# Performance work log

Measured on AMD Instinct MI355X. Metric: run time of the kernel, lower is better.

## Reference

```python
import jax, jax.numpy as jnp
import numpy as np

B, A, D = 1024, 200, 128
H = 8
DH = D // H
TANH_CLIP = 10.0


def setup_inputs() -> dict:
    key = jax.random.key(0)
    k = jax.random.split(key, 8)
    agent_embd = jax.random.normal(k[0], (B, A, D), dtype=jnp.float32)
    # old_action must be a permutation per row (no revisits under the mask)
    old_action = jax.vmap(lambda kk: jax.random.permutation(kk, A))(
        jax.random.split(k[1], B)).astype(jnp.int32)
    s = 0.02
    W_placeholder = jax.random.uniform(k[2], (D,), jnp.float32, -1.0, 1.0)
    W_node = jax.random.normal(k[3], (D, 3 * D), jnp.float32) * s   # project_node_embeddings
    W_fixed = jax.random.normal(k[4], (D, D), jnp.float32) * s      # project_fixed_context
    W_step = jax.random.normal(k[5], (D, D), jnp.float32) * s       # project_step_context
    W_out = jax.random.normal(k[6], (D, D), jnp.float32) * s        # project_out
    return {"agent_embd": agent_embd, "old_action": old_action,
            "W_placeholder": W_placeholder, "W_node": W_node,
            "W_fixed": W_fixed, "W_step": W_step, "W_out": W_out}


def _decode(agent_embd, old_action, W_placeholder, W_node, W_fixed, W_step, W_out):
    b_, a_, d_ = agent_embd.shape
    inv_sqrt_dh = np.float32(1.0 / np.sqrt(DH))
    inv_sqrt_d = np.float32(1.0 / np.sqrt(d_))
    batch_ix = jnp.arange(b_)

    # _precompute: fixed context + per-head K/V + logit keys
    graph_embed = agent_embd.mean(axis=1)                      # [B, D]
    fixed_ctx = graph_embed @ W_fixed                          # [B, D]
    proj = agent_embd @ W_node                                 # [B, A, 3D]
    gK, gV, logit_K = jnp.split(proj, 3, axis=-1)              # each [B, A, D]
    gK = gK.reshape(b_, a_, H, DH).transpose(2, 0, 1, 3)       # [H, B, A, dh]
    gV = gV.reshape(b_, a_, H, DH).transpose(2, 0, 1, 3)       # [H, B, A, dh]

    def step(carry, xs):
        mask, prev = carry                                     # [B, A] bool, [B] int
        i, act = xs
        gathered = agent_embd[batch_ix, prev]                  # [B, D]
        step_ctx = jnp.where(i == 0, W_placeholder[None, :], gathered)
        query = fixed_ctx + step_ctx @ W_step                  # [B, D]
        mask = jnp.where(i > 0, mask.at[batch_ix, prev].set(True), mask)

        Q = query.reshape(b_, H, DH).transpose(1, 0, 2)        # [H, B, dh]
        compat = jnp.einsum('hbd,hbad->hba', Q, gK) * inv_sqrt_dh
        compat = jnp.where(mask[None, :, :], -jnp.inf, compat)  # mask_inner
        attn = jax.nn.softmax(compat, axis=-1)                 # [H, B, A]
        heads = jnp.einsum('hba,hbad->hbd', attn, gV)          # [H, B, dh]
        glimpse = heads.transpose(1, 0, 2).reshape(b_, d_) @ W_out  # [B, D]

        logits = jnp.einsum('bd,bad->ba', glimpse, logit_K) * inv_sqrt_d
        logits = jnp.tanh(logits) * TANH_CLIP
        logits = jnp.where(mask, -jnp.inf, logits)             # mask_logits
        log_p = jax.nn.log_softmax(logits, axis=-1)            # [B, A]
        lp_sel = log_p[batch_ix, act]                          # [B]
        return (mask, act), lp_sel

    mask0 = jnp.zeros((b_, a_), dtype=bool)
    prev0 = jnp.zeros((b_,), dtype=old_action.dtype)
    xs = (jnp.arange(a_), old_action.T)
    _, lps = jax.lax.scan(step, (mask0, prev0), xs)            # lps: [A, B]
    return old_action, lps.sum(axis=0)


def reference(agent_embd, old_action, W_placeholder, W_node, W_fixed, W_step, W_out):
    return _decode(agent_embd, old_action, W_placeholder, W_node, W_fixed, W_step, W_out)
```

## Files before the change

### kernel.cpp

```cpp
#include <hip/hip_runtime.h>
#include <cstdint>
#include <cstddef>

#define BB 1024
#define AA 200
#define DD 128
#define HH 8
#define N3 384

typedef unsigned short u16;
typedef unsigned int u32;
typedef __attribute__((ext_vector_type(8))) short bf16x8;
typedef __attribute__((ext_vector_type(4))) float f32x4;

__device__ __forceinline__ float bf2f(u16 v){ return __uint_as_float(((u32)v) << 16); }
__device__ __forceinline__ u16 f2bf(float f){
  u32 u = __float_as_uint(f);
  u32 r = u + 0x7fffu + ((u >> 16) & 1u);
  return (u16)(r >> 16);
}
__device__ __forceinline__ u32 pack2(float lo, float hi){
  return (u32)f2bf(lo) | ((u32)f2bf(hi) << 16);
}
__device__ __forceinline__ u32 pack2t(float lo, float hi){
  return (__float_as_uint(hi) & 0xFFFF0000u) | (__float_as_uint(lo) >> 16);
}
__device__ __forceinline__ bf16x8 pack8(float4 a, float4 b){
  bf16x8 o;
  o[0] = (short)f2bf(a.x); o[1] = (short)f2bf(a.y);
  o[2] = (short)f2bf(a.z); o[3] = (short)f2bf(a.w);
  o[4] = (short)f2bf(b.x); o[5] = (short)f2bf(b.y);
  o[6] = (short)f2bf(b.z); o[7] = (short)f2bf(b.w);
  return o;
}

__global__ void k_act_rank(const int* __restrict__ oa, float* __restrict__ out0,
                           int* __restrict__ rank){
  int m = blockIdx.x * 256 + threadIdx.x;
  if (m >= BB*AA) return;
  int v = oa[m];
  out0[m] = (float)v;
  int b = m / AA;
  int j = m - b*AA;
  rank[b*AA + v] = j;
}

__global__ void k_prep(const float* __restrict__ Wn, const float* __restrict__ Ws,
                       const float* __restrict__ Wo,
                       u16* __restrict__ WnT, u16* __restrict__ WsT,
                       u16* __restrict__ WoT){
  int idx = blockIdx.x * 256 + threadIdx.x;
  if (idx < 49152){
    int n = idx >> 7, k = idx & 127;
    WnT[idx] = f2bf(Wn[k*N3 + n]);
  } else if (idx < 65536){
    int j = idx - 49152;
    int n = j >> 7, k = j & 127;
    WsT[j] = f2bf(Ws[k*DD + n]);
  } else if (idx < 81920){
    int j = idx - 65536;
    int n = j >> 7, k = j & 127;
    WoT[j] = f2bf(Wo[k*DD + n]);
  }
}

__global__ void k_fixed(const float* __restrict__ E, const float* __restrict__ Wf,
                        float* __restrict__ fixedc){
  int b = blockIdx.x;
  int d = threadIdx.x;
  __shared__ float ge[DD];
  const float* Eb = E + (size_t)b*AA*DD;
  float s = 0.f;
  for (int a = 0; a < AA; ++a) s += Eb[a*DD + d];
  ge[d] = s * (1.0f/AA);
  __syncthreads();
  float acc = 0.f;
  for (int k = 0; k < DD; ++k) acc = fmaf(ge[k], Wf[k*DD + d], acc);
  fixedc[b*DD + d] = acc;
}

__global__ __launch_bounds__(256) void k_proj_mfma(const float* __restrict__ E,
                                                   const u16* __restrict__ WnT,
                                                   u16* __restrict__ proj){
  const int t = threadIdx.x;
  const int w = t >> 6, L = t & 63;
  const int l16 = L & 15, lq = L >> 4;
  const int m0 = blockIdx.x * 128;
  const int n0 = blockIdx.y * 128;
  const int row0 = m0 + w*32;

  f32x4 acc[2][8] = {};
  const float* Arow0 = E + (size_t)(row0 + l16)*DD;
  const float* Arow1 = Arow0 + (size_t)16*DD;
  #pragma unroll
  for (int ks = 0; ks < 4; ++ks){
    int ko = ks*32 + lq*8;
    bf16x8 a0 = pack8(*(const float4*)(Arow0 + ko), *(const float4*)(Arow0 + ko + 4));
    bf16x8 a1 = pack8(*(const float4*)(Arow1 + ko), *(const float4*)(Arow1 + ko + 4));
    #pragma unroll
    for (int nt = 0; nt < 8; ++nt){
      union { uint4 u; bf16x8 v; } bb;
      bb.u = *(const uint4*)(WnT + (size_t)(n0 + nt*16 + l16)*DD + ko);
      acc[0][nt] = __builtin_amdgcn_mfma_f32_16x16x32_bf16(a0, bb.v, acc[0][nt], 0, 0, 0);
      acc[1][nt] = __builtin_amdgcn_mfma_f32_16x16x32_bf16(a1, bb.v, acc[1][nt], 0, 0, 0);
    }
  }
  #pragma unroll
  for (int mt = 0; mt < 2; ++mt)
    #pragma unroll
    for (int r = 0; r < 4; ++r){
      int row = row0 + mt*16 + lq*4 + r;
      u16* dst = proj + (size_t)row*N3 + n0;
      #pragma unroll
      for (int nt = 0; nt < 8; ++nt)
        dst[nt*16 + l16] = f2bf(acc[mt][nt][r]);
    }
}

__global__ __launch_bounds__(256) void k_query_mfma(const float* __restrict__ E,
                                                    const int* __restrict__ oa,
                                                    const float* __restrict__ Wp,
                                                    const u16* __restrict__ WsT,
                                                    const float* __restrict__ fixedc,
                                                    u16* __restrict__ qhg){
  const int t = threadIdx.x;
  const int w = t >> 6, L = t & 63;
  const int l16 = L & 15, lq = L >> 4;
  const int m0 = blockIdx.x * 128;
  const int row0 = m0 + w*32;

  const float* src[2];
  #pragma unroll
  for (int mt = 0; mt < 2; ++mt){
    int q = row0 + mt*16 + l16;
    int b = q / AA, i = q - b*AA;
    src[mt] = (i == 0) ? Wp : (E + (size_t)(b*AA + oa[b*AA + i - 1])*DD);
  }

  f32x4 acc[2][8] = {};
  #pragma unroll
  for (int ks = 0; ks < 4; ++ks){
    int ko = ks*32 + lq*8;
    bf16x8 a0 = pack8(*(const float4*)(src[0] + ko), *(const float4*)(src[0] + ko + 4));
    bf16x8 a1 = pack8(*(const float4*)(src[1] + ko), *(const float4*)(src[1] + ko + 4));
    #pragma unroll
    for (int nt = 0; nt < 8; ++nt){
      union { uint4 u; bf16x8 v; } bb;
      bb.u = *(const uint4*)(WsT + (size_t)(nt*16 + l16)*DD + ko);
      acc[0][nt] = __builtin_amdgcn_mfma_f32_16x16x32_bf16(a0, bb.v, acc[0][nt], 0, 0, 0);
      acc[1][nt] = __builtin_amdgcn_mfma_f32_16x16x32_bf16(a1, bb.v, acc[1][nt], 0, 0, 0);
    }
  }
  #pragma unroll
  for (int mt = 0; mt < 2; ++mt)
    #pragma unroll
    for (int r = 0; r < 4; ++r){
      int row = row0 + mt*16 + lq*4 + r;
      int b = row / AA;
      const float* fc = fixedc + (size_t)b*DD;
      u16* dst = qhg + (size_t)row*DD;
      #pragma unroll
      for (int nt = 0; nt < 8; ++nt)
        dst[nt*16 + l16] = f2bf((acc[mt][nt][r] + fc[nt*16 + l16]) * 0.25f);
    }
}

#define KSTR 24
#define VSTR 232
template<int IT>
__device__ __forceinline__ void attn_tile(const u16* KL, const u16* VT,
                                          u16* Qbase, int l16, int lq,
                                          bool dm0, bool dm1, bool dm2, bool dm3){
  constexpr int NT = 13 - IT;
  const int qi = IT*16 + l16;
  const float NEG_INF = -__builtin_inff();

  union { uint4 u; bf16x8 v; } qf8;
  qf8.u.x = 0; qf8.u.y = 0; qf8.u.z = 0; qf8.u.w = 0;
  if (qi < AA){
    uint2 q2 = *(const uint2*)(Qbase + (size_t)qi*DD + lq*4);
    qf8.u.x = q2.x; qf8.u.y = q2.y;
  }

  f32x4 S[NT];
  #pragma unroll
  for (int k = 0; k < NT; ++k){
    const int at = IT + k;
    union { uint4 u; bf16x8 v; } kf8;
    uint2 k2 = *(const uint2*)&KL[(at*16 + l16)*KSTR + lq*4];
    kf8.u.x = k2.x; kf8.u.y = k2.y; kf8.u.z = 0; kf8.u.w = 0;
    f32x4 z = {0.f,0.f,0.f,0.f};
    S[k] = __builtin_amdgcn_mfma_f32_16x16x32_bf16(kf8.v, qf8.v, z, 0, 0, 0);
  }
  S[0][0] = dm0 ? NEG_INF : S[0][0];
  S[0][1] = dm1 ? NEG_INF : S[0][1];
  S[0][2] = dm2 ? NEG_INF : S[0][2];
  S[0][3] = dm3 ? NEG_INF : S[0][3];
  if (lq >= 2){
    S[NT-1][0] = NEG_INF; S[NT-1][1] = NEG_INF;
    S[NT-1][2] = NEG_INF; S[NT-1][3] = NEG_INF;
  }
  float m = fmaxf(fmaxf(S[0][0], S[0][1]), fmaxf(S[0][2], S[0][3]));
  #pragma unroll
  for (int k = 1; k < NT; ++k)
    m = fmaxf(m, fmaxf(fmaxf(S[k][0], S[k][1]), fmaxf(S[k][2], S[k][3])));
  m = fmaxf(m, __shfl_xor(m, 16));
  m = fmaxf(m, __shfl_xor(m, 32));
  m = fmaxf(m, -1e30f);
  float s0 = 0.f, s1 = 0.f, s2 = 0.f, s3 = 0.f;
  #pragma unroll
  for (int k = 0; k < NT; ++k){
    float e0 = __expf(S[k][0] - m);
    float e1 = __expf(S[k][1] - m);
    float e2 = __expf(S[k][2] - m);
    float e3 = __expf(S[k][3] - m);
    S[k][0] = e0; S[k][1] = e1; S[k][2] = e2; S[k][3] = e3;
    s0 += e0; s1 += e1; s2 += e2; s3 += e3;
  }
  float sum = (s0 + s1) + (s2 + s3);
  sum += __shfl_xor(sum, 16);
  sum += __shfl_xor(sum, 32);
  float inv = 1.0f / sum;
  f32x4 acc = {0.f,0.f,0.f,0.f};
  #pragma unroll
  for (int k = 0; k < NT; ++k){
    const int at = IT + k;
    union { uint4 u; bf16x8 v; } pa8, vb8;
    pa8.u.x = pack2t(S[k][0], S[k][1]);
    pa8.u.y = pack2t(S[k][2], S[k][3]);
    pa8.u.z = 0; pa8.u.w = 0;
    uint2 v2 = *(const uint2*)&VT[l16*VSTR + at*16 + lq*4];
    vb8.u.x = v2.x; vb8.u.y = v2.y; vb8.u.z = 0; vb8.u.w = 0;
    acc = __builtin_amdgcn_mfma_f32_16x16x32_bf16(vb8.v, pa8.v, acc, 0, 0, 0);
  }
  if (qi < AA){
    uint2 ov;
    ov.x = pack2(acc[0]*inv, acc[1]*inv);
    ov.y = pack2(acc[2]*inv, acc[3]*inv);
    *(uint2*)(Qbase + (size_t)qi*DD + lq*4) = ov;
  }
}

__global__ __launch_bounds__(256) void k_attn(const u16* __restrict__ proj,
                                              const int* __restrict__ oa,
                                              u16* __restrict__ qhg){
  __shared__ __align__(16) u16 KL[208*KSTR];
  __shared__ __align__(16) u16 VT[16*VSTR];
  const int b = blockIdx.x;
  const int h = blockIdx.y;
  const int t = threadIdx.x;
  const int w = t >> 6, L = t & 63;
  const int l16 = L & 15, lq = L >> 4;

  if (t < 192) KL[200*KSTR + t] = 0;
  if (t < 128){ int d = t >> 3, c = t & 7; VT[d*VSTR + 200 + c] = 0; }

  if (t < AA){
    int a = oa[(size_t)b*AA + t];
    const u16* src = proj + ((size_t)(b*AA + a))*N3 + h*16;
    uint4 k0 = *(const uint4*)(src);
    uint4 k1 = *(const uint4*)(src + 8);
    *(uint4*)&KL[t*KSTR]     = k0;
    *(uint4*)&KL[t*KSTR + 8] = k1;
    const u16* sv = src + 128;
    u16 d16[16];
    *(uint4*)(d16)   = *(const uint4*)(sv);
    *(uint4*)(d16+8) = *(const uint4*)(sv+8);
    #pragma unroll
    for (int d = 0; d < 16; ++d) VT[d*VSTR + t] = d16[d];
  }
  __syncthreads();

  u16* Qbase = qhg + (size_t)b*AA*DD + h*16;
  const bool dm0 = (lq*4 + 0) < l16;
  const bool dm1 = (lq*4 + 1) < l16;
  const bool dm2 = (lq*4 + 2) < l16;
  const bool dm3 = (lq*4 + 3) < l16;

  if (w == 0){
    attn_tile<0>(KL, VT, Qbase, l16, lq, dm0, dm1, dm2, dm3);
    attn_tile<3>(KL, VT, Qbase, l16, lq, dm0, dm1, dm2, dm3);
  } else if (w == 1){
    attn_tile<1>(KL, VT, Qbase, l16, lq, dm0, dm1, dm2, dm3);
    attn_tile<2>(KL, VT, Qbase, l16, lq, dm0, dm1, dm2, dm3);
  } else if (w == 2){
    attn_tile<4>(KL, VT, Qbase, l16, lq, dm0, dm1, dm2, dm3);
    attn_tile<6>(KL, VT, Qbase, l16, lq, dm0, dm1, dm2, dm3);
    attn_tile<8>(KL, VT, Qbase, l16, lq, dm0, dm1, dm2, dm3);
    attn_tile<10>(KL, VT, Qbase, l16, lq, dm0, dm1, dm2, dm3);
    attn_tile<12>(KL, VT, Qbase, l16, lq, dm0, dm1, dm2, dm3);
  } else {
    attn_tile<5>(KL, VT, Qbase, l16, lq, dm0, dm1, dm2, dm3);
    attn_tile<7>(KL, VT, Qbase, l16, lq, dm0, dm1, dm2, dm3);
    attn_tile<9>(KL, VT, Qbase, l16, lq, dm0, dm1, dm2, dm3);
    attn_tile<11>(KL, VT, Qbase, l16, lq, dm0, dm1, dm2, dm3);
  }
}

__global__ __launch_bounds__(256) void k_glimpse_mfma(const u16* __restrict__ qhg,
                                                      const u16* __restrict__ WoT,
                                                      u16* __restrict__ proj){
  const int t = threadIdx.x;
  const int w = t >> 6, L = t & 63;
  const int l16 = L & 15, lq = L >> 4;
  const int m0 = blockIdx.x * 128;
  const int row0 = m0 + w*32;

  f32x4 acc[2][8] = {};
  const u16* Arow0 = qhg + (size_t)(row0 + l16)*DD;
  const u16* Arow1 = Arow0 + (size_t)16*DD;
  #pragma unroll
  for (int ks = 0; ks < 4; ++ks){
    int ko = ks*32 + lq*8;
    union { uint4 u; bf16x8 v; } a0, a1;
    a0.u = *(const uint4*)(Arow0 + ko);
    a1.u = *(const uint4*)(Arow1 + ko);
    #pragma unroll
    for (int nt = 0; nt < 8; ++nt){
      union { uint4 u; bf16x8 v; } bb;
      bb.u = *(const uint4*)(WoT + (size_t)(nt*16 + l16)*DD + ko);
      acc[0][nt] = __builtin_amdgcn_mfma_f32_16x16x32_bf16(a0.v, bb.v, acc[0][nt], 0, 0, 0);
      acc[1][nt] = __builtin_amdgcn_mfma_f32_16x16x32_bf16(a1.v, bb.v, acc[1][nt], 0, 0, 0);
    }
  }
  #pragma unroll
  for (int mt = 0; mt < 2; ++mt)
    #pragma unroll
    for (int r = 0; r < 4; ++r){
      int row = row0 + mt*16 + lq*4 + r;
      u16* dst = proj + (size_t)row*N3;
      #pragma unroll
      for (int nt = 0; nt < 8; ++nt)
        dst[nt*16 + l16] = f2bf(acc[mt][nt][r]);
    }
}

__global__ __launch_bounds__(256) void k_logits(const u16* __restrict__ proj,
                                                const int* __restrict__ rank,
                                                const int* __restrict__ oa,
                                                float* __restrict__ outlps){
  __shared__ float red[4];
  const int b = blockIdx.x;
  const int t = threadIdx.x;
  const int w = t >> 6, L = t & 63;
  const int l16 = L & 15, lq = L >> 4;
  const float inv_sqrt_d = 0.08838834764831843f;

  const u16* Gbase  = proj + (size_t)b*AA*N3;
  const u16* LKbase = Gbase + 256;

  int ra[13];
  #pragma unroll
  for (int at = 0; at < 13; ++at){
    int a = at*16 + l16;
    ra[at] = (a < AA) ? rank[b*AA + a] : -1;
  }

  float lp_part = 0.f;

  for (int it = w; it < 13; it += 4){
    bf16x8 af[4];
    {
      const u16* arow = Gbase + (size_t)(it*16 + l16)*N3;
      #pragma unroll
      for (int kb = 0; kb < 4; ++kb){
        union { uint4 u; bf16x8 v; } tmp;
        tmp.u = *(const uint4*)(arow + kb*32 + lq*8);
        af[kb] = tmp.v;
      }
    }
    f32x4 S[13];
    #pragma unroll
    for (int at = 0; at < 13; ++at){
      const u16* brow = LKbase + (size_t)(at*16 + l16)*N3;
      f32x4 acc = {0.f,0.f,0.f,0.f};
      #pragma unroll
      for (int kb = 0; kb < 4; ++kb){
        union { uint4 u; bf16x8 v; } tmp;
        tmp.u = *(const uint4*)(brow + kb*32 + lq*8);
        acc = __builtin_amdgcn_mfma_f32_16x16x32_bf16(af[kb], tmp.v, acc, 0, 0, 0);
      }
      S[at] = acc;
    }
    #pragma unroll
    for (int at = 0; at < 13; ++at)
      #pragma unroll
      for (int r = 0; r < 4; ++r){
        int i = it*16 + lq*4 + r;
        float x = S[at][r] * inv_sqrt_d;
        float e = __expf(2.0f*x);
        float th = 1.0f - 2.0f/(e + 1.0f);
        S[at][r] = (ra[at] < i) ? -__builtin_inff() : 10.0f*th;
      }
    #pragma unroll
    for (int r = 0; r < 4; ++r){
      int i = it*16 + lq*4 + r;
      float m = S[0][r];
      #pragma unroll
      for (int at = 1; at < 13; ++at) m = fmaxf(m, S[at][r]);
      #pragma unroll
      for (int off = 1; off < 16; off <<= 1) m = fmaxf(m, __shfl_xor(m, off));
      float sum = 0.f;
      #pragma unroll
      for (int at = 0; at < 13; ++at) sum += __expf(S[at][r] - m);
      #pragma unroll
      for (int off = 1; off < 16; off <<= 1) sum += __shfl_xor(sum, off);
      if (i < AA){
        float lse = m + __logf(sum);
        int act = oa[b*AA + i];
        if ((act & 15) == l16){
          int at0 = act >> 4;
          #pragma unroll
          for (int at = 0; at < 13; ++at)
            if (at == at0) lp_part += S[at][r] - lse;
        }
      }
    }
  }
  #pragma unroll
  for (int off = 1; off < 64; off <<= 1) lp_part += __shfl_xor(lp_part, off);
  if (L == 0) red[w] = lp_part;
  __syncthreads();
  if (t == 0) outlps[b] = red[0] + red[1] + red[2] + red[3];
}

extern "C" void kernel_launch(void* const* d_in, const int* in_sizes, int n_in,
                              void* d_out, int out_size, void* d_ws, size_t ws_size,
                              hipStream_t stream){
  const float* E  = (const float*)d_in[0];
  const int*   oa = (const int*)d_in[1];
  const float* Wp = (const float*)d_in[2];
  const float* Wn = (const float*)d_in[3];
  const float* Wf = (const float*)d_in[4];
  const float* Ws = (const float*)d_in[5];
  const float* Wo = (const float*)d_in[6];
  float* out = (float*)d_out;

  char* ws = (char*)d_ws;
  int*   rank   = (int*)ws;
  float* fixedc = (float*)(ws + 819200);
  u16*   proj   = (u16*)(ws + 1343488);
  u16*   qhg    = (u16*)(ws + 158629888);
  u16*   WnT    = (u16*)(ws + 211058688);
  u16*   WsT    = (u16*)(ws + 211156992);
  u16*   WoT    = (u16*)(ws + 211189760);

  k_act_rank<<<dim3((BB*AA)/256), 256, 0, stream>>>(oa, out, rank);
  k_prep<<<dim3(320), 256, 0, stream>>>(Wn, Ws, Wo, WnT, WsT, WoT);
  k_fixed<<<dim3(BB), 128, 0, stream>>>(E, Wf, fixedc);
  k_proj_mfma<<<dim3((BB*AA)/128, N3/128), 256, 0, stream>>>(E, WnT, proj);
  k_query_mfma<<<dim3((BB*AA)/128), 256, 0, stream>>>(E, oa, Wp, WsT, fixedc, qhg);
  k_attn<<<dim3(BB, HH), 256, 0, stream>>>(proj, oa, qhg);
  k_glimpse_mfma<<<dim3((BB*AA)/128), 256, 0, stream>>>(qhg, WoT, proj);
  k_logits<<<dim3(BB), 256, 0, stream>>>(proj, rank, oa, out + BB*AA);
}
```

Baseline: 649.1 us.

## Restructure node projection GEMM to cover all outputs per block with vectorized stores

The node projection kernel now has each block handle 64 rows across all 384 output columns. The MFMA operands are swapped (weights as A, activations as B), so each lane holds four consecutive output columns and can write them as one packed 8-byte store instead of scattered 2-byte stores. Each E row is read once per block rather than once per column tile. The fixed-context kernel now splits the mean over agents across two thread halves to double its parallelism, at the cost of recomputing the combined mean inside the inner loop.

```diff
diff --git a/kernel.cpp b/kernel.cpp
--- a/kernel.cpp
+++ b/kernel.cpp
@@ -67,16 +67,25 @@
 __global__ void k_fixed(const float* __restrict__ E, const float* __restrict__ Wf,
                         float* __restrict__ fixedc){
   int b = blockIdx.x;
-  int d = threadIdx.x;
-  __shared__ float ge[DD];
-  const float* Eb = E + (size_t)b*AA*DD;
+  int t = threadIdx.x;
+  int half = t >> 7, d = t & 127;
+  __shared__ float ge[2][DD];
+  const float* Eb = E + (size_t)b*AA*DD + (size_t)half*100*DD;
   float s = 0.f;
-  for (int a = 0; a < AA; ++a) s += Eb[a*DD + d];
-  ge[d] = s * (1.0f/AA);
+  #pragma unroll 4
+  for (int a = 0; a < 100; ++a) s += Eb[a*DD + d];
+  ge[half][d] = s;
   __syncthreads();
-  float acc = 0.f;
-  for (int k = 0; k < DD; ++k) acc = fmaf(ge[k], Wf[k*DD + d], acc);
-  fixedc[b*DD + d] = acc;
+  if (t < DD){
+    float g = (ge[0][t] + ge[1][t]) * (1.0f/AA);
+    float acc = 0.f;
+    for (int k = 0; k < DD; ++k){
+      float gk = (ge[0][k] + ge[1][k]) * (1.0f/AA);
+      acc = fmaf(gk, Wf[k*DD + t], acc);
+    }
+    (void)g;
+    fixedc[b*DD + t] = acc;
+  }
 }
 
 __global__ __launch_bounds__(256) void k_proj_mfma(const float* __restrict__ E,
@@ -85,36 +94,33 @@
   const int t = threadIdx.x;
   const int w = t >> 6, L = t & 63;
   const int l16 = L & 15, lq = L >> 4;
-  const int m0 = blockIdx.x * 128;
-  const int n0 = blockIdx.y * 128;
-  const int row0 = m0 + w*32;
-
-  f32x4 acc[2][8] = {};
-  const float* Arow0 = E + (size_t)(row0 + l16)*DD;
-  const float* Arow1 = Arow0 + (size_t)16*DD;
-  #pragma unroll
-  for (int ks = 0; ks < 4; ++ks){
-    int ko = ks*32 + lq*8;
-    bf16x8 a0 = pack8(*(const float4*)(Arow0 + ko), *(const float4*)(Arow0 + ko + 4));
-    bf16x8 a1 = pack8(*(const float4*)(Arow1 + ko), *(const float4*)(Arow1 + ko + 4));
+  const int row = blockIdx.x * 64 + w*16 + l16;
+  const float* Erow = E + (size_t)row*DD;
+  u16* dst = proj + (size_t)row*N3;
+
+  #pragma unroll
+  for (int c = 0; c < 3; ++c){
+    const int n0 = c*128;
+    f32x4 acc[8] = {};
+    #pragma unroll
+    for (int ks = 0; ks < 4; ++ks){
+      int ko = ks*32 + lq*8;
+      bf16x8 bfrag = pack8(*(const float4*)(Erow + ko), *(const float4*)(Erow + ko + 4));
+      #pragma unroll
+      for (int nt = 0; nt < 8; ++nt){
+        union { uint4 u; bf16x8 v; } aa;
+        aa.u = *(const uint4*)(WnT + (size_t)(n0 + nt*16 + l16)*DD + ko);
+        acc[nt] = __builtin_amdgcn_mfma_f32_16x16x32_bf16(aa.v, bfrag, acc[nt], 0, 0, 0);
+      }
+    }
     #pragma unroll
     for (int nt = 0; nt < 8; ++nt){
-      union { uint4 u; bf16x8 v; } bb;
-      bb.u = *(const uint4*)(WnT + (size_t)(n0 + nt*16 + l16)*DD + ko);
-      acc[0][nt] = __builtin_amdgcn_mfma_f32_16x16x32_bf16(a0, bb.v, acc[0][nt], 0, 0, 0);
-      acc[1][nt] = __builtin_amdgcn_mfma_f32_16x16x32_bf16(a1, bb.v, acc[1][nt], 0, 0, 0);
-    }
-  }
-  #pragma unroll
-  for (int mt = 0; mt < 2; ++mt)
-    #pragma unroll
-    for (int r = 0; r < 4; ++r){
-      int row = row0 + mt*16 + lq*4 + r;
-      u16* dst = proj + (size_t)row*N3 + n0;
-      #pragma unroll
-      for (int nt = 0; nt < 8; ++nt)
-        dst[nt*16 + l16] = f2bf(acc[mt][nt][r]);
-    }
+      uint2 ov;
+      ov.x = pack2(acc[nt][0], acc[nt][1]);
+      ov.y = pack2(acc[nt][2], acc[nt][3]);
+      *(uint2*)(dst + n0 + nt*16 + lq*4) = ov;
+    }
+  }
 }
 
 __global__ __launch_bounds__(256) void k_query_mfma(const float* __restrict__ E,
@@ -447,8 +453,8 @@
 
   k_act_rank<<<dim3((BB*AA)/256), 256, 0, stream>>>(oa, out, rank);
   k_prep<<<dim3(320), 256, 0, stream>>>(Wn, Ws, Wo, WnT, WsT, WoT);
-  k_fixed<<<dim3(BB), 128, 0, stream>>>(E, Wf, fixedc);
-  k_proj_mfma<<<dim3((BB*AA)/128, N3/128), 256, 0, stream>>>(E, WnT, proj);
+  k_fixed<<<dim3(BB), 256, 0, stream>>>(E, Wf, fixedc);
+  k_proj_mfma<<<dim3((BB*AA)/64), 256, 0, stream>>>(E, WnT, proj);
   k_query_mfma<<<dim3((BB*AA)/128), 256, 0, stream>>>(E, oa, Wp, WsT, fixedc, qhg);
   k_attn<<<dim3(BB, HH), 256, 0, stream>>>(proj, oa, qhg);
   k_glimpse_mfma<<<dim3((BB*AA)/128), 256, 0, stream>>>(qhg, WoT, proj);
```

Result: slower. 726.8 us (+12.0%).
